# Performance work log

Measured on AMD Instinct MI355X. Metric: run time of the kernel, lower is better.

The kernel has to match this reference:

```python
import jax, jax.numpy as jnp
import numpy as np
import math

B, L, D, H, DFF = 8, 2048, 512, 8, 2048
FACTOR = 5

def setup_inputs() -> dict:
    key = jax.random.key(0)
    ks = jax.random.split(key, 20)
    r = lambda k, shape, s=0.02: (jax.random.normal(k, shape, jnp.float32) * s)
    return {
        'encoder_output': jax.random.normal(ks[0], (B, L, D), jnp.float32),
        'Wq': r(ks[1], (D, D)), 'bq': jnp.zeros((D,), jnp.float32),
        'Wk': r(ks[2], (D, D)), 'bk': jnp.zeros((D,), jnp.float32),
        'Wv': r(ks[3], (D, D)), 'bv': jnp.zeros((D,), jnp.float32),
        'Wo': r(ks[4], (D, D)), 'bo': jnp.zeros((D,), jnp.float32),
        'W1': r(ks[5], (DFF, D)), 'b1': jnp.zeros((DFF,), jnp.float32),
        'W2': r(ks[6], (D, DFF)), 'b2': jnp.zeros((D,), jnp.float32),
        'g1': jnp.ones((D,), jnp.float32), 'be1': jnp.zeros((D,), jnp.float32),
        'g2': jnp.ones((D,), jnp.float32), 'be2': jnp.zeros((D,), jnp.float32),
        'Wout': r(ks[7], (D, 1)), 'bout': jnp.zeros((1,), jnp.float32),
    }

def _layernorm(x, g, b, eps=1e-5):
    m = x.mean(-1, keepdims=True)
    v = x.var(-1, keepdims=True)
    return (x - m) / jnp.sqrt(v + eps) * g + b

def reference(encoder_output, Wq, bq, Wk, bk, Wv, bv, Wo, bo,
              W1, b1, W2, b2, g1, be1, g2, be2, Wout, bout):
    x = encoder_output  # [B, L, D]
    dh = D // H
    u = min(L, FACTOR * math.ceil(math.log(L)))  # number of active queries (static)

    # multi-head projections -> [B, H, L, dh]
    q = (x @ Wq + bq).reshape(B, L, H, dh).transpose(0, 2, 1, 3)
    k = (x @ Wk + bk).reshape(B, L, H, dh).transpose(0, 2, 1, 3)
    v = (x @ Wv + bv).reshape(B, L, H, dh).transpose(0, 2, 1, 3)

    # deterministic prob-sparse: sparsity measurement over all keys
    scores = jnp.einsum('bhld,bhsd->bhls', q, k) / math.sqrt(dh)  # [B,H,L,L]
    M = scores.max(-1) - scores.mean(-1)                           # [B,H,L]
    top_idx = jax.lax.top_k(M, u)[1]                               # [B,H,u]

    top_scores = jnp.take_along_axis(scores, top_idx[..., None], axis=2)  # [B,H,u,L]
    attn = jax.nn.softmax(top_scores, axis=-1)
    top_out = jnp.einsum('bhus,bhsd->bhud', attn, v)               # [B,H,u,dh]

    # lazy queries get mean(V); active queries get true attention
    ctx = jnp.broadcast_to(v.mean(axis=2, keepdims=True), (B, H, L, dh))
    bi = jnp.arange(B)[:, None, None]
    hi = jnp.arange(H)[None, :, None]
    ctx = ctx.at[bi, hi, top_idx].set(top_out)                     # [B,H,L,dh]

    attn_out = ctx.transpose(0, 2, 1, 3).reshape(B, L, D) @ Wo + bo  # [B,L,D]

    # decoder body: mean-pool, residual norms, pointwise conv FFN (eval-mode dropout = identity)
    a = attn_out.mean(axis=1)                 # [B, D]
    a = _layernorm(a + a, g1, be1)[:, None, :]  # [B, 1, D]  (a + dropout(a))

    ff = jax.nn.relu(a @ W1.T + b1)           # conv1d k=1 == linear, [B,1,DFF]
    ff = ff @ W2.T + b2                       # [B,1,D]
    out = _layernorm(a + ff, g2, be2)         # [B,1,D]

    forecasts = (out @ Wout + bout).squeeze(-1)  # [B,1]
    return forecasts, out
```

## Files before the change

### kernel.cpp

```cpp
#include <hip/hip_runtime.h>
#include <hip/hip_bf16.h>


#define B_   8
#define L_   2048
#define D_   512
#define H_   8
#define DH_  64
#define DFF_ 2048
#define U_   40
#define BH_  64
#define NM_  16384
#define NCK_ 16
#define CKS_ 128

typedef __bf16 bf16_t;
typedef __bf16 bf16x8 __attribute__((ext_vector_type(8)));
typedef float  f32x4  __attribute__((ext_vector_type(4)));

__device__ __forceinline__ void gl_lds16(const bf16_t* g, bf16_t* l) {
    __builtin_amdgcn_global_load_lds(
        (const __attribute__((address_space(1))) unsigned int*)g,
        (__attribute__((address_space(3))) unsigned int*)l, 16, 0, 0);
}

__global__ void k_cvt(const float* __restrict__ X, bf16_t* __restrict__ Xb) {
    size_t g = (size_t)blockIdx.x * 256 + threadIdx.x;
    const float4* xp = (const float4*)&X[g * 8];
    float4 f0 = xp[0], f1 = xp[1];
    bf16x8 hv;
    hv[0]=(bf16_t)f0.x; hv[1]=(bf16_t)f0.y; hv[2]=(bf16_t)f0.z; hv[3]=(bf16_t)f0.w;
    hv[4]=(bf16_t)f1.x; hv[5]=(bf16_t)f1.y; hv[6]=(bf16_t)f1.z; hv[7]=(bf16_t)f1.w;
    *(bf16x8*)&Xb[g * 8] = hv;
}

__global__ void k_transpose_w(const float* __restrict__ Wq, const float* __restrict__ Wk,
                              const float* __restrict__ Wv, bf16_t* __restrict__ WT) {
    __shared__ float tile[64][65];
    int blk = blockIdx.x;
    int mat = blk >> 6, tl = blk & 63;
    int tr = (tl >> 3) << 6;
    int tc = (tl & 7) << 6;
    const float* W = (mat == 0) ? Wq : (mat == 1) ? Wk : Wv;
    int t = threadIdx.x;
    #pragma unroll
    for (int i = 0; i < 16; ++i) {
        int e = t + i * 256, r = e >> 6, c = e & 63;
        tile[r][c] = W[(size_t)(tr + r) * 512 + tc + c];
    }
    __syncthreads();
    #pragma unroll
    for (int i = 0; i < 16; ++i) {
        int e = t + i * 256, r = e >> 6, c = e & 63;
        WT[(size_t)(mat * 512 + tc + r) * 512 + tr + c] = (bf16_t)tile[c][r];
    }
}

__global__ __launch_bounds__(256) void k_qkv(const bf16_t* __restrict__ Xb,
        const bf16_t* __restrict__ WT,
        const float* __restrict__ bq, const float* __restrict__ bk, const float* __restrict__ bv,
        bf16_t* __restrict__ Qb, bf16_t* __restrict__ Kb, float* __restrict__ Vf) {
    __shared__ bf16_t As[128 * 64];
    __shared__ bf16_t Bs[128 * 64];
    int t = threadIdx.x;
    int m0 = blockIdx.y * 128;
    int n0 = blockIdx.x * 128;
    int wv = t >> 6, lane = t & 63, lr = lane & 15, qd = lane >> 4;
    int wm = (wv & 1) * 64, wn = (wv >> 1) * 64;
    f32x4 acc[4][4];
    #pragma unroll
    for (int a = 0; a < 4; ++a)
        #pragma unroll
        for (int b = 0; b < 4; ++b) acc[a][b] = (f32x4){0.f, 0.f, 0.f, 0.f};

    for (int kt = 0; kt < 8; ++kt) {
        __syncthreads();
        #pragma unroll
        for (int i = 0; i < 4; ++i) {
            int ch = i * 256 + t, r = ch >> 3, c8 = ch & 7;
            gl_lds16(&Xb[(size_t)(m0 + r) * 512 + kt * 64 + c8 * 8], &As[ch * 8]);
        }
        #pragma unroll
        for (int i = 0; i < 4; ++i) {
            int ch = i * 256 + t, r = ch >> 3, c8 = ch & 7;
            gl_lds16(&WT[(size_t)(n0 + r) * 512 + kt * 64 + c8 * 8], &Bs[ch * 8]);
        }
        __syncthreads();
        bf16x8 af[4][2], bfg[4][2];
        #pragma unroll
        for (int rf = 0; rf < 4; ++rf)
            #pragma unroll
            for (int ks = 0; ks < 2; ++ks)
                af[rf][ks] = *(bf16x8*)&As[(wm + rf * 16 + lr) * 64 + ks * 32 + qd * 8];
        #pragma unroll
        for (int cf = 0; cf < 4; ++cf)
            #pragma unroll
            for (int ks = 0; ks < 2; ++ks)
                bfg[cf][ks] = *(bf16x8*)&Bs[(wn + cf * 16 + lr) * 64 + ks * 32 + qd * 8];
        #pragma unroll
        for (int cf = 0; cf < 4; ++cf)
            #pragma unroll
            for (int rf = 0; rf < 4; ++rf) {
                acc[rf][cf] = __builtin_amdgcn_mfma_f32_16x16x32_bf16(af[rf][0], bfg[cf][0], acc[rf][cf], 0, 0, 0);
                acc[rf][cf] = __builtin_amdgcn_mfma_f32_16x16x32_bf16(af[rf][1], bfg[cf][1], acc[rf][cf], 0, 0, 0);
            }
    }
    int sec = n0 >> 9;
    const float* bias = (sec == 0) ? bq : (sec == 1) ? bk : bv;
    #pragma unroll
    for (int rf = 0; rf < 4; ++rf) {
        #pragma unroll
        for (int r = 0; r < 4; ++r) {
            int m = m0 + wm + rf * 16 + qd * 4 + r;
            int b = m >> 11, l = m & 2047;
            #pragma unroll
            for (int cf = 0; cf < 4; ++cf) {
                int n = n0 + wn + cf * 16 + lr;
                int nn = n & 511;
                int h = nn >> 6, d = nn & 63;
                float val = acc[rf][cf][r] + bias[nn];
                size_t oidx = ((size_t)(b * 8 + h) * L_ + l) * 64 + d;
                if (sec == 0)      Qb[oidx] = (bf16_t)val;
                else if (sec == 1) Kb[oidx] = (bf16_t)val;
                else               Vf[oidx] = val;
            }
        }
    }
}

__global__ __launch_bounds__(256) void k_rowmax(const bf16_t* __restrict__ Qb,
        const bf16_t* __restrict__ Kb, float* __restrict__ rowmax) {
    __shared__ bf16_t Ks[128 * 64];
    int t = threadIdx.x;
    int bh = blockIdx.y;
    int row0 = blockIdx.x * 256;
    int wv = t >> 6, lane = t & 63, lr = lane & 15, qd = lane >> 4;
    size_t base = (size_t)bh * L_ * DH_;
    bf16x8 af[4][2];
    #pragma unroll
    for (int rf = 0; rf < 4; ++rf)
        #pragma unroll
        for (int ks = 0; ks < 2; ++ks)
            af[rf][ks] = *(const bf16x8*)&Qb[base + (size_t)(row0 + wv * 64 + rf * 16 + lr) * 64 + ks * 32 + qd * 8];
    float pmax[4][4];
    #pragma unroll
    for (int a = 0; a < 4; ++a)
        #pragma unroll
        for (int r = 0; r < 4; ++r) pmax[a][r] = -3.4e38f;

    for (int cb = 0; cb < 16; ++cb) {
        __syncthreads();
        #pragma unroll
        for (int i = 0; i < 4; ++i) {
            int ch = i * 256 + t, r = ch >> 3, c8 = ch & 7;
            gl_lds16(&Kb[base + (size_t)(cb * 128 + r) * 64 + c8 * 8], &Ks[ch * 8]);
        }
        __syncthreads();
        #pragma unroll
        for (int cf = 0; cf < 8; cf += 2) {
            bf16x8 bA0 = *(bf16x8*)&Ks[(cf * 16 + lr) * 64 + qd * 8];
            bf16x8 bA1 = *(bf16x8*)&Ks[(cf * 16 + lr) * 64 + 32 + qd * 8];
            bf16x8 bB0 = *(bf16x8*)&Ks[((cf + 1) * 16 + lr) * 64 + qd * 8];
            bf16x8 bB1 = *(bf16x8*)&Ks[((cf + 1) * 16 + lr) * 64 + 32 + qd * 8];
            #pragma unroll
            for (int rf = 0; rf < 4; ++rf) {
                f32x4 z = {0.f, 0.f, 0.f, 0.f};
                f32x4 c0 = __builtin_amdgcn_mfma_f32_16x16x32_bf16(af[rf][0], bA0, z, 0, 0, 0);
                c0 = __builtin_amdgcn_mfma_f32_16x16x32_bf16(af[rf][1], bA1, c0, 0, 0, 0);
                f32x4 c1 = __builtin_amdgcn_mfma_f32_16x16x32_bf16(af[rf][0], bB0, z, 0, 0, 0);
                c1 = __builtin_amdgcn_mfma_f32_16x16x32_bf16(af[rf][1], bB1, c1, 0, 0, 0);
                #pragma unroll
                for (int r = 0; r < 4; ++r)
                    pmax[rf][r] = fmaxf(pmax[rf][r], fmaxf(c0[r], c1[r]));
            }
        }
    }
    #pragma unroll
    for (int rf = 0; rf < 4; ++rf)
        #pragma unroll
        for (int r = 0; r < 4; ++r) {
            float v = pmax[rf][r];
            v = fmaxf(v, __shfl_xor(v, 1));
            v = fmaxf(v, __shfl_xor(v, 2));
            v = fmaxf(v, __shfl_xor(v, 4));
            v = fmaxf(v, __shfl_xor(v, 8));
            if (lr == 0)
                rowmax[bh * L_ + row0 + wv * 64 + rf * 16 + qd * 4 + r] = v;
        }
}

__global__ void k_sums(const bf16_t* __restrict__ Kb, const float* __restrict__ Vf,
                       float* __restrict__ kpart, float* __restrict__ vpart) {
    __shared__ float red[32][64];
    int t = threadIdx.x;
    int seg = blockIdx.x, bh = blockIdx.y;
    int d8 = t & 7, g = t >> 3;
    size_t base = (size_t)bh * L_ * DH_ + (size_t)seg * 256 * DH_;
    float s[8];
    #pragma unroll
    for (int j = 0; j < 8; ++j) s[j] = 0.f;
    #pragma unroll
    for (int ss = 0; ss < 8; ++ss) {
        bf16x8 kk = *(const bf16x8*)&Kb[base + (size_t)(g * 8 + ss) * 64 + d8 * 8];
        #pragma unroll
        for (int j = 0; j < 8; ++j) s[j] += (float)kk[j];
    }
    #pragma unroll
    for (int j = 0; j < 8; ++j) red[g][d8 * 8 + j] = s[j];
    __syncthreads();
    if (t < 64) {
        float a = 0.f;
        #pragma unroll
        for (int gg = 0; gg < 32; ++gg) a += red[gg][t];
        kpart[(bh * 8 + seg) * 64 + t] = a;
    }
    __syncthreads();
    #pragma unroll
    for (int j = 0; j < 8; ++j) s[j] = 0.f;
    #pragma unroll
    for (int ss = 0; ss < 8; ++ss) {
        const float4* vp = (const float4*)&Vf[base + (size_t)(g * 8 + ss) * 64 + d8 * 8];
        float4 v0 = vp[0], v1 = vp[1];
        s[0]+=v0.x; s[1]+=v0.y; s[2]+=v0.z; s[3]+=v0.w;
        s[4]+=v1.x; s[5]+=v1.y; s[6]+=v1.z; s[7]+=v1.w;
    }
    __syncthreads();
    #pragma unroll
    for (int j = 0; j < 8; ++j) red[g][d8 * 8 + j] = s[j];
    __syncthreads();
    if (t < 64) {
        float a = 0.f;
        #pragma unroll
        for (int gg = 0; gg < 32; ++gg) a += red[gg][t];
        vpart[(bh * 8 + seg) * 64 + t] = a;
    }
}

__global__ void k_M(const bf16_t* __restrict__ Qb, const float* __restrict__ rowmax,
                    const float* __restrict__ kpart, float* __restrict__ Mv) {
    __shared__ float ks_s[64];
    int t = threadIdx.x, blk = blockIdx.x;
    int bh = blk >> 3, lb = blk & 7;
    if (t < 64) {
        float a = 0.f;
        #pragma unroll
        for (int seg = 0; seg < 8; ++seg) a += kpart[(bh * 8 + seg) * 64 + t];
        ks_s[t] = a;
    }
    __syncthreads();
    int l = lb * 256 + t;
    const bf16x8* qp = (const bf16x8*)&Qb[((size_t)bh * L_ + l) * 64];
    float acc = 0.f;
    #pragma unroll
    for (int c8 = 0; c8 < 8; ++c8) {
        bf16x8 q8 = qp[c8];
        #pragma unroll
        for (int j = 0; j < 8; ++j) acc += (float)q8[j] * ks_s[c8 * 8 + j];
    }
    Mv[bh * L_ + l] = rowmax[bh * L_ + l] - acc * (1.0f / 2048.0f);
}

__global__ void k_topk(const float* __restrict__ Mv, int* __restrict__ topidx) {
    int lane = threadIdx.x;
    int bh = blockIdx.x;
    unsigned key[32];
    #pragma unroll
    for (int j = 0; j < 32; ++j) {
        unsigned b = __float_as_uint(Mv[bh * L_ + j * 64 + lane]);
        key[j] = (b & 0x80000000u) ? ~b : (b | 0x80000000u);
    }
    unsigned lo = 0u, hi = 0xFFFFFFFFu;
    while (lo < hi) {
        unsigned mid = lo + ((hi - lo) >> 1) + 1;
        int c = 0;
        #pragma unroll
        for (int j = 0; j < 32; ++j)
            c += __popcll(__ballot(key[j] >= mid));
        if (c >= U_) lo = mid; else hi = mid - 1;
    }
    unsigned K40 = lo;
    int c_gt = 0;
    #pragma unroll
    for (int j = 0; j < 32; ++j)
        c_gt += __popcll(__ballot(key[j] > K40));
    unsigned long long lmask = (1ull << lane) - 1ull;
    int base_gt = 0, base_eq = 0;
    #pragma unroll
    for (int j = 0; j < 32; ++j) {
        bool gt = key[j] > K40, eq = key[j] == K40;
        unsigned long long mg = __ballot(gt);
        unsigned long long me = __ballot(eq);
        if (gt) {
            int pos = base_gt + __popcll(mg & lmask);
            topidx[bh * U_ + pos] = j * 64 + lane;
        } else if (eq) {
            int ep = base_eq + __popcll(me & lmask);
            if (c_gt + ep < U_)
                topidx[bh * U_ + c_gt + ep] = j * 64 + lane;
        }
        base_gt += __popcll(mg);
        base_eq += __popcll(me);
    }
}

__global__ __launch_bounds__(256) void k_attn2(const bf16_t* __restrict__ Qb,
        const bf16_t* __restrict__ Kb, const float* __restrict__ Vf,
        const int* __restrict__ topidx, float* __restrict__ part) {
    __shared__ bf16_t Qs[48 * 72];
    __shared__ bf16_t Ks[128 * 64];
    __shared__ bf16_t Vt[64 * 136];
    __shared__ float  wred[4][48];
    __shared__ float  frow[48];
    __shared__ int    tid_s[40];
    bf16_t* Ps = Ks;

    int t = threadIdx.x;
    int ck = blockIdx.x, bh = blockIdx.y;
    int c0 = ck * CKS_;
    size_t base = (size_t)bh * L_ * DH_;
    if (t < 40) tid_s[t] = topidx[bh * U_ + t];
    __syncthreads();
    #pragma unroll
    for (int i = 0; i < 4; ++i) {
        int s = i * 256 + t, r = s >> 3, cs = s & 7, c = cs ^ (r & 7);
        gl_lds16(&Kb[base + (size_t)(c0 + r) * 64 + c * 8], &Ks[s * 8]);
    }
    for (int e = t; e < 48 * 8; e += 256) {
        int r = e >> 3, c8 = e & 7;
        bf16x8 v;
        #pragma unroll
        for (int j = 0; j < 8; ++j) v[j] = (bf16_t)0.f;
        if (r < 40) v = *(const bf16x8*)&Qb[base + (size_t)tid_s[r] * 64 + c8 * 8];
        *(bf16x8*)&Qs[r * 72 + c8 * 8] = v;
    }
    #pragma unroll
    for (int i = 0; i < 8; ++i) {
        int e = t + i * 256;
        int key = e >> 4, d4 = e & 15;
        float4 v = *(const float4*)&Vf[base + (size_t)(c0 + key) * 64 + d4 * 4];
        Vt[(d4 * 4 + 0) * 136 + key] = (bf16_t)v.x;
        Vt[(d4 * 4 + 1) * 136 + key] = (bf16_t)v.y;
        Vt[(d4 * 4 + 2) * 136 + key] = (bf16_t)v.z;
        Vt[(d4 * 4 + 3) * 136 + key] = (bf16_t)v.w;
    }
    __syncthreads();

    int wv = t >> 6, lane = t & 63, lr = lane & 15, qd = lane >> 4;
    bf16x8 aq[3][2];
    #pragma unroll
    for (int tm = 0; tm < 3; ++tm)
        #pragma unroll
        for (int ks = 0; ks < 2; ++ks)
            aq[tm][ks] = *(bf16x8*)&Qs[(tm * 16 + lr) * 72 + ks * 32 + qd * 8];
    f32x4 S[3][2];
    #pragma unroll
    for (int nt = 0; nt < 2; ++nt) {
        int key = wv * 32 + nt * 16 + lr;
        bf16x8 bk0 = *(bf16x8*)&Ks[key * 64 + ((qd ^ (key & 7)) * 8)];
        bf16x8 bk1 = *(bf16x8*)&Ks[key * 64 + (((4 + qd) ^ (key & 7)) * 8)];
        #pragma unroll
        for (int tm = 0; tm < 3; ++tm) {
            f32x4 z = {0.f, 0.f, 0.f, 0.f};
            z = __builtin_amdgcn_mfma_f32_16x16x32_bf16(aq[tm][0], bk0, z, 0, 0, 0);
            S[tm][nt] = __builtin_amdgcn_mfma_f32_16x16x32_bf16(aq[tm][1], bk1, z, 0, 0, 0);
        }
    }
    float rm[3][4];
    #pragma unroll
    for (int tm = 0; tm < 3; ++tm)
        #pragma unroll
        for (int r = 0; r < 4; ++r) {
            float v = fmaxf(S[tm][0][r], S[tm][1][r]);
            v = fmaxf(v, __shfl_xor(v, 1));
            v = fmaxf(v, __shfl_xor(v, 2));
            v = fmaxf(v, __shfl_xor(v, 4));
            v = fmaxf(v, __shfl_xor(v, 8));
            rm[tm][r] = v;
        }
    if (lr == 0) {
        #pragma unroll
        for (int tm = 0; tm < 3; ++tm)
            #pragma unroll
            for (int r = 0; r < 4; ++r)
                wred[wv][tm * 16 + qd * 4 + r] = rm[tm][r];
    }
    __syncthreads();
    if (t < 48)
        frow[t] = fmaxf(fmaxf(wred[0][t], wred[1][t]), fmaxf(wred[2][t], wred[3][t]));
    __syncthreads();
    float rs_[3][4];
    #pragma unroll
    for (int tm = 0; tm < 3; ++tm) {
        #pragma unroll
        for (int r = 0; r < 4; ++r) {
            float fm = frow[tm * 16 + qd * 4 + r];
            float s0 = __expf((S[tm][0][r] - fm) * 0.125f);
            float s1 = __expf((S[tm][1][r] - fm) * 0.125f);
            Ps[(tm * 16 + qd * 4 + r) * 136 + wv * 32 + lr]      = (bf16_t)s0;
            Ps[(tm * 16 + qd * 4 + r) * 136 + wv * 32 + 16 + lr] = (bf16_t)s1;
            rs_[tm][r] = s0 + s1;
        }
    }
    #pragma unroll
    for (int tm = 0; tm < 3; ++tm)
        #pragma unroll
        for (int r = 0; r < 4; ++r) {
            float v = rs_[tm][r];
            v += __shfl_xor(v, 1);
            v += __shfl_xor(v, 2);
            v += __shfl_xor(v, 4);
            v += __shfl_xor(v, 8);
            rs_[tm][r] = v;
        }
    if (lr == 0) {
        #pragma unroll
        for (int tm = 0; tm < 3; ++tm)
            #pragma unroll
            for (int r = 0; r < 4; ++r)
                wred[wv][tm * 16 + qd * 4 + r] = rs_[tm][r];
    }
    __syncthreads();
    float* pb = &part[(((size_t)bh * NCK_ + ck) * 40) * 66];
    if (t < 40) {
        pb[t * 66 + 64] = frow[t] * 0.125f;
        pb[t * 66 + 65] = wred[0][t] + wred[1][t] + wred[2][t] + wred[3][t];
    }
    f32x4 O[3];
    #pragma unroll
    for (int tm = 0; tm < 3; ++tm) O[tm] = (f32x4){0.f, 0.f, 0.f, 0.f};
    #pragma unroll
    for (int kk = 0; kk < 4; ++kk) {
        bf16x8 bv = *(bf16x8*)&Vt[(wv * 16 + lr) * 136 + kk * 32 + qd * 8];
        #pragma unroll
        for (int tm = 0; tm < 3; ++tm) {
            bf16x8 ap = *(bf16x8*)&Ps[(tm * 16 + lr) * 136 + kk * 32 + qd * 8];
            O[tm] = __builtin_amdgcn_mfma_f32_16x16x32_bf16(ap, bv, O[tm], 0, 0, 0);
        }
    }
    #pragma unroll
    for (int tm = 0; tm < 3; ++tm)
        #pragma unroll
        for (int r = 0; r < 4; ++r) {
            int row = tm * 16 + qd * 4 + r;
            if (row < 40) pb[row * 66 + wv * 16 + lr] = O[tm][r];
        }
}

__global__ void k_attnred(const float* __restrict__ part, float* __restrict__ tout) {
    int t = threadIdx.x, bh = blockIdx.x;
    int d = t & 63, rg = t >> 6;
    const float* pb0 = &part[((size_t)bh * NCK_) * 40 * 66];
    for (int ri = 0; ri < 10; ++ri) {
        int r = rg + 4 * ri;
        float M = -3.4e38f;
        #pragma unroll
        for (int c = 0; c < NCK_; ++c) M = fmaxf(M, pb0[(c * 40 + r) * 66 + 64]);
        float lsum = 0.f, osum = 0.f;
        #pragma unroll
        for (int c = 0; c < NCK_; ++c) {
            float w = __expf(pb0[(c * 40 + r) * 66 + 64] - M);
            lsum += w * pb0[(c * 40 + r) * 66 + 65];
            osum += w * pb0[(c * 40 + r) * 66 + d];
        }
        tout[((size_t)bh * U_ + r) * 64 + d] = osum / lsum;
    }
}

__global__ void k_ctx(const float* __restrict__ vpart, const float* __restrict__ topout,
                      const float* __restrict__ Wo, const float* __restrict__ bo,
                      const float* __restrict__ g1, const float* __restrict__ be1,
                      float* __restrict__ a2) {
    __shared__ float cm[512];
    __shared__ float rs[256], rq[256];
    int t = threadIdx.x, b = blockIdx.x;
    #pragma unroll
    for (int p = 0; p < 2; ++p) {
        int hd = t + p * 256;
        int h = hd >> 6, dd = hd & 63;
        int bh = b * 8 + h;
        float vs = 0.f;
        #pragma unroll
        for (int seg = 0; seg < 8; ++seg) vs += vpart[(bh * 8 + seg) * 64 + dd];
        float tsum = 0.f;
        for (int ii = 0; ii < U_; ++ii) tsum += topout[((size_t)bh * U_ + ii) * 64 + dd];
        cm[hd] = (0.98046875f * vs + tsum) * (1.0f / 2048.0f);
    }
    __syncthreads();
    float x[2];
    #pragma unroll
    for (int p = 0; p < 2; ++p) {
        int j = t + p * 256;
        float acc = bo[j];
        for (int c = 0; c < 128; ++c) {
            float4 cv = *(const float4*)&cm[c * 4];
            acc += cv.x * Wo[(size_t)(c * 4 + 0) * 512 + j];
            acc += cv.y * Wo[(size_t)(c * 4 + 1) * 512 + j];
            acc += cv.z * Wo[(size_t)(c * 4 + 2) * 512 + j];
            acc += cv.w * Wo[(size_t)(c * 4 + 3) * 512 + j];
        }
        x[p] = 2.0f * acc;
    }
    rs[t] = x[0] + x[1];
    rq[t] = x[0] * x[0] + x[1] * x[1];
    __syncthreads();
    for (int str = 128; str > 0; str >>= 1) {
        if (t < str) { rs[t] += rs[t + str]; rq[t] += rq[t + str]; }
        __syncthreads();
    }
    float mean = rs[0] * (1.0f / 512.0f);
    float var  = rq[0] * (1.0f / 512.0f) - mean * mean;
    float rstd = rsqrtf(var + 1e-5f);
    #pragma unroll
    for (int p = 0; p < 2; ++p) {
        int j = t + p * 256;
        a2[b * 512 + j] = (x[p] - mean) * rstd * g1[j] + be1[j];
    }
}

__global__ void k_ff1p(const float* __restrict__ a2, const float* __restrict__ W1,
                       float* __restrict__ ffp) {
    __shared__ float Ws[64 * 132];
    __shared__ float as[8 * 128];
    int t = threadIdx.x;
    int jb = blockIdx.x, seg = blockIdx.y;
    int j0 = jb * 64, c0 = seg * 128;
    #pragma unroll
    for (int i = 0; i < 8; ++i) {
        int e = t + i * 256;
        int r = e >> 5, c4 = e & 31;
        *(float4*)&Ws[r * 132 + c4 * 4] =
            *(const float4*)&W1[(size_t)(j0 + r) * 512 + c0 + c4 * 4];
    }
    for (int e = t; e < 1024; e += 256) {
        int b = e >> 7, c = e & 127;
        as[b * 128 + c] = a2[b * 512 + c0 + c];
    }
    __syncthreads();
    int j = t & 63, bp = t >> 6;
    float acc0 = 0.f, acc1 = 0.f;
    for (int c = 0; c < 32; ++c) {
        float4 w  = *(float4*)&Ws[j * 132 + c * 4];
        float4 xa = *(float4*)&as[(bp * 2) * 128 + c * 4];
        float4 xb = *(float4*)&as[(bp * 2 + 1) * 128 + c * 4];
        acc0 += w.x * xa.x + w.y * xa.y + w.z * xa.z + w.w * xa.w;
        acc1 += w.x * xb.x + w.y * xb.y + w.z * xb.z + w.w * xb.w;
    }
    ffp[(size_t)(seg * 8 + bp * 2) * 2048 + j0 + j]     = acc0;
    ffp[(size_t)(seg * 8 + bp * 2 + 1) * 2048 + j0 + j] = acc1;
}

__global__ void k_ffr(const float* __restrict__ ffp, const float* __restrict__ b1v,
                      float* __restrict__ ffb) {
    int e = blockIdx.x * 256 + threadIdx.x;
    int b = e >> 11, j = e & 2047;
    float s = b1v[j];
    #pragma unroll
    for (int seg = 0; seg < 4; ++seg) s += ffp[(size_t)(seg * 8 + b) * 2048 + j];
    ffb[b * 2048 + j] = fmaxf(s, 0.f);
}

__global__ void k_ff2p(const float* __restrict__ ffb, const float* __restrict__ W2,
                       float* __restrict__ ff2p) {
    __shared__ float Ws[32 * 260];
    __shared__ float fs[8 * 256];
    int t = threadIdx.x;
    int db = blockIdx.x, seg = blockIdx.y;
    int d0 = db * 32, c0 = seg * 256;
    #pragma unroll
    for (int i = 0; i < 8; ++i) {
        int e = t + i * 256;
        int r = e >> 6, c4 = e & 63;
        *(float4*)&Ws[r * 260 + c4 * 4] =
            *(const float4*)&W2[(size_t)(d0 + r) * 2048 + c0 + c4 * 4];
    }
    for (int e = t; e < 2048; e += 256) {
        int b = e >> 8, c = e & 255;
        fs[b * 256 + c] = ffb[b * 2048 + c0 + c];
    }
    __syncthreads();
    int d = t & 31, b = t >> 5;
    float acc = 0.f;
    for (int c = 0; c < 64; ++c) {
        float4 w = *(float4*)&Ws[d * 260 + c * 4];
        float4 x = *(float4*)&fs[b * 256 + c * 4];
        acc += w.x * x.x + w.y * x.y + w.z * x.z + w.w * x.w;
    }
    ff2p[(size_t)(seg * 8 + b) * 512 + d0 + d] = acc;
}

__global__ void k_final(const float* __restrict__ a2, const float* __restrict__ ff2p,
                        const float* __restrict__ b2v,
                        const float* __restrict__ g2, const float* __restrict__ be2,
                        const float* __restrict__ Wout, const float* __restrict__ bout,
                        float* __restrict__ dout) {
    __shared__ float rs[256], rq[256];
    int t = threadIdx.x, b = blockIdx.x;
    float f0 = b2v[t], f1 = b2v[t + 256];
    #pragma unroll
    for (int seg = 0; seg < 8; ++seg) {
        f0 += ff2p[(size_t)(seg * 8 + b) * 512 + t];
        f1 += ff2p[(size_t)(seg * 8 + b) * 512 + t + 256];
    }
    float x0 = a2[b * 512 + t] + f0;
    float x1 = a2[b * 512 + t + 256] + f1;
    rs[t] = x0 + x1;
    rq[t] = x0 * x0 + x1 * x1;
    __syncthreads();
    for (int str = 128; str > 0; str >>= 1) {
        if (t < str) { rs[t] += rs[t + str]; rq[t] += rq[t + str]; }
        __syncthreads();
    }
    float mean = rs[0] * (1.0f / 512.0f);
    float var  = rq[0] * (1.0f / 512.0f) - mean * mean;
    float rstd = rsqrtf(var + 1e-5f);
    float o0 = (x0 - mean) * rstd * g2[t]       + be2[t];
    float o1 = (x1 - mean) * rstd * g2[t + 256] + be2[t + 256];
    dout[8 + b * 512 + t]       = o0;
    dout[8 + b * 512 + t + 256] = o1;
    __syncthreads();
    rs[t] = o0 * Wout[t] + o1 * Wout[t + 256];
    __syncthreads();
    for (int str = 128; str > 0; str >>= 1) {
        if (t < str) rs[t] += rs[t + str];
        __syncthreads();
    }
    if (t == 0) dout[b] = rs[0] + bout[0];
}

extern "C" void kernel_launch(void* const* d_in, const int* in_sizes, int n_in,
                              void* d_out, int out_size, void* d_ws, size_t ws_size,
                              hipStream_t stream) {
    const float* X    = (const float*)d_in[0];
    const float* Wq   = (const float*)d_in[1];
    const float* bq   = (const float*)d_in[2];
    const float* Wk   = (const float*)d_in[3];
    const float* bk   = (const float*)d_in[4];
    const float* Wv   = (const float*)d_in[5];
    const float* bv   = (const float*)d_in[6];
    const float* Wo   = (const float*)d_in[7];
    const float* bo   = (const float*)d_in[8];
    const float* W1   = (const float*)d_in[9];
    const float* b1   = (const float*)d_in[10];
    const float* W2   = (const float*)d_in[11];
    const float* b2   = (const float*)d_in[12];
    const float* g1   = (const float*)d_in[13];
    const float* be1  = (const float*)d_in[14];
    const float* g2   = (const float*)d_in[15];
    const float* be2  = (const float*)d_in[16];
    const float* Wout = (const float*)d_in[17];
    const float* bout = (const float*)d_in[18];
    float* out = (float*)d_out;

    char* ws = (char*)d_ws;
    size_t off = 0;
    auto alloc = [&](size_t bytes) -> void* {
        void* p = ws + off;
        off += (bytes + 255) & ~(size_t)255;
        return p;
    };
    bf16_t* Xb   = (bf16_t*)alloc((size_t)NM_ * D_ * 2);
    bf16_t* WT   = (bf16_t*)alloc((size_t)1536 * 512 * 2);
    bf16_t* Qb   = (bf16_t*)alloc((size_t)BH_ * L_ * DH_ * 2);
    bf16_t* Kb   = (bf16_t*)alloc((size_t)BH_ * L_ * DH_ * 2);
    float*  Vf   = (float*) alloc((size_t)BH_ * L_ * DH_ * 4);
    float*  rmx  = (float*) alloc((size_t)BH_ * L_ * 4);
    float*  Mv   = (float*) alloc((size_t)BH_ * L_ * 4);
    float*  kpart= (float*) alloc((size_t)BH_ * 8 * 64 * 4);
    float*  vpart= (float*) alloc((size_t)BH_ * 8 * 64 * 4);
    int*    tidx = (int*)   alloc((size_t)BH_ * U_ * 4);
    float*  tout = (float*) alloc((size_t)BH_ * U_ * 64 * 4);
    float*  a2   = (float*) alloc(8 * 512 * 4);
    float*  ffp  = (float*) alloc((size_t)4 * 8 * 2048 * 4);
    float*  ffb  = (float*) alloc(8 * 2048 * 4);
    float*  ff2p = (float*) alloc((size_t)8 * 8 * 512 * 4);
    float*  part = (float*)Xb;
    (void)ws_size; (void)in_sizes; (void)n_in; (void)out_size;

    hipLaunchKernelGGL(k_cvt,         dim3(4096),       dim3(256), 0, stream, X, Xb);
    hipLaunchKernelGGL(k_transpose_w, dim3(192),        dim3(256), 0, stream, Wq, Wk, Wv, WT);
    hipLaunchKernelGGL(k_qkv,         dim3(12, 128),    dim3(256), 0, stream, Xb, WT, bq, bk, bv, Qb, Kb, Vf);
    hipLaunchKernelGGL(k_rowmax,      dim3(8, 64),      dim3(256), 0, stream, Qb, Kb, rmx);
    hipLaunchKernelGGL(k_sums,        dim3(8, 64),      dim3(256), 0, stream, Kb, Vf, kpart, vpart);
    hipLaunchKernelGGL(k_M,           dim3(512),        dim3(256), 0, stream, Qb, rmx, kpart, Mv);
    hipLaunchKernelGGL(k_topk,        dim3(64),         dim3(64),  0, stream, Mv, tidx);
    hipLaunchKernelGGL(k_attn2,       dim3(NCK_, 64),   dim3(256), 0, stream, Qb, Kb, Vf, tidx, part);
    hipLaunchKernelGGL(k_attnred,     dim3(64),         dim3(256), 0, stream, part, tout);
    hipLaunchKernelGGL(k_ctx,         dim3(8),          dim3(256), 0, stream, vpart, tout, Wo, bo, g1, be1, a2);
    hipLaunchKernelGGL(k_ff1p,        dim3(32, 4),      dim3(256), 0, stream, a2, W1, ffp);
    hipLaunchKernelGGL(k_ffr,         dim3(64),         dim3(256), 0, stream, ffp, b1, ffb);
    hipLaunchKernelGGL(k_ff2p,        dim3(16, 8),      dim3(256), 0, stream, ffb, W2, ff2p);
    hipLaunchKernelGGL(k_final,       dim3(8),          dim3(256), 0, stream, a2, ff2p, b2, g2, be2, Wout, bout, out);
}
```

Before: 320.1 us.

## Fuse sparsity measure into rowmax kernel, swizzle K LDS, halve rows per block

```diff
diff --git a/kernel.cpp b/kernel.cpp
--- a/kernel.cpp
+++ b/kernel.cpp
@@ -129,22 +129,44 @@
 }
 
 __global__ __launch_bounds__(256) void k_rowmax(const bf16_t* __restrict__ Qb,
-        const bf16_t* __restrict__ Kb, float* __restrict__ rowmax) {
+        const bf16_t* __restrict__ Kb, const float* __restrict__ kpart,
+        float* __restrict__ Mv) {
     __shared__ bf16_t Ks[128 * 64];
+    __shared__ float ksum_s[64];
+    __shared__ float dot_s[128];
     int t = threadIdx.x;
     int bh = blockIdx.y;
-    int row0 = blockIdx.x * 256;
+    int row0 = blockIdx.x * 128;
     int wv = t >> 6, lane = t & 63, lr = lane & 15, qd = lane >> 4;
     size_t base = (size_t)bh * L_ * DH_;
-    bf16x8 af[4][2];
-    #pragma unroll
-    for (int rf = 0; rf < 4; ++rf)
+    if (t < 64) {
+        float a = 0.f;
+        #pragma unroll
+        for (int seg = 0; seg < 8; ++seg) a += kpart[(bh * 8 + seg) * 64 + t];
+        ksum_s[t] = a;
+    }
+    bf16x8 af[2][2];
+    #pragma unroll
+    for (int rf = 0; rf < 2; ++rf)
         #pragma unroll
         for (int ks = 0; ks < 2; ++ks)
-            af[rf][ks] = *(const bf16x8*)&Qb[base + (size_t)(row0 + wv * 64 + rf * 16 + lr) * 64 + ks * 32 + qd * 8];
-    float pmax[4][4];
-    #pragma unroll
-    for (int a = 0; a < 4; ++a)
+            af[rf][ks] = *(const bf16x8*)&Qb[base + (size_t)(row0 + wv * 32 + rf * 16 + lr) * 64 + ks * 32 + qd * 8];
+    __syncthreads();
+    #pragma unroll
+    for (int rf = 0; rf < 2; ++rf) {
+        float v = 0.f;
+        #pragma unroll
+        for (int ks = 0; ks < 2; ++ks)
+            #pragma unroll
+            for (int j = 0; j < 8; ++j)
+                v += (float)af[rf][ks][j] * ksum_s[ks * 32 + qd * 8 + j];
+        v += __shfl_xor(v, 16);
+        v += __shfl_xor(v, 32);
+        if (qd == 0) dot_s[wv * 32 + rf * 16 + lr] = v;
+    }
+    float pmax[2][4];
+    #pragma unroll
+    for (int a = 0; a < 2; ++a)
         #pragma unroll
         for (int r = 0; r < 4; ++r) pmax[a][r] = -3.4e38f;
 
@@ -152,18 +174,19 @@
         __syncthreads();
         #pragma unroll
         for (int i = 0; i < 4; ++i) {
-            int ch = i * 256 + t, r = ch >> 3, c8 = ch & 7;
-            gl_lds16(&Kb[base + (size_t)(cb * 128 + r) * 64 + c8 * 8], &Ks[ch * 8]);
+            int s = i * 256 + t, r = s >> 3, cs = s & 7, c = cs ^ (r & 7);
+            gl_lds16(&Kb[base + (size_t)(cb * 128 + r) * 64 + c * 8], &Ks[s * 8]);
         }
         __syncthreads();
         #pragma unroll
         for (int cf = 0; cf < 8; cf += 2) {
-            bf16x8 bA0 = *(bf16x8*)&Ks[(cf * 16 + lr) * 64 + qd * 8];
-            bf16x8 bA1 = *(bf16x8*)&Ks[(cf * 16 + lr) * 64 + 32 + qd * 8];
-            bf16x8 bB0 = *(bf16x8*)&Ks[((cf + 1) * 16 + lr) * 64 + qd * 8];
-            bf16x8 bB1 = *(bf16x8*)&Ks[((cf + 1) * 16 + lr) * 64 + 32 + qd * 8];
-            #pragma unroll
-            for (int rf = 0; rf < 4; ++rf) {
+            int keyA = cf * 16 + lr, keyB = (cf + 1) * 16 + lr;
+            bf16x8 bA0 = *(bf16x8*)&Ks[keyA * 64 + ((qd ^ (keyA & 7)) * 8)];
+            bf16x8 bA1 = *(bf16x8*)&Ks[keyA * 64 + (((4 + qd) ^ (keyA & 7)) * 8)];
+            bf16x8 bB0 = *(bf16x8*)&Ks[keyB * 64 + ((qd ^ (keyB & 7)) * 8)];
+            bf16x8 bB1 = *(bf16x8*)&Ks[keyB * 64 + (((4 + qd) ^ (keyB & 7)) * 8)];
+            #pragma unroll
+            for (int rf = 0; rf < 2; ++rf) {
                 f32x4 z = {0.f, 0.f, 0.f, 0.f};
                 f32x4 c0 = __builtin_amdgcn_mfma_f32_16x16x32_bf16(af[rf][0], bA0, z, 0, 0, 0);
                 c0 = __builtin_amdgcn_mfma_f32_16x16x32_bf16(af[rf][1], bA1, c0, 0, 0, 0);
@@ -176,7 +199,7 @@
         }
     }
     #pragma unroll
-    for (int rf = 0; rf < 4; ++rf)
+    for (int rf = 0; rf < 2; ++rf)
         #pragma unroll
         for (int r = 0; r < 4; ++r) {
             float v = pmax[rf][r];
@@ -184,8 +207,10 @@
             v = fmaxf(v, __shfl_xor(v, 2));
             v = fmaxf(v, __shfl_xor(v, 4));
             v = fmaxf(v, __shfl_xor(v, 8));
-            if (lr == 0)
-                rowmax[bh * L_ + row0 + wv * 64 + rf * 16 + qd * 4 + r] = v;
+            if (lr == 0) {
+                int row = wv * 32 + rf * 16 + qd * 4 + r;
+                Mv[bh * L_ + row0 + row] = v - dot_s[row] * (1.0f / 2048.0f);
+            }
         }
 }
 
@@ -234,30 +259,6 @@
         for (int gg = 0; gg < 32; ++gg) a += red[gg][t];
         vpart[(bh * 8 + seg) * 64 + t] = a;
     }
-}
-
-__global__ void k_M(const bf16_t* __restrict__ Qb, const float* __restrict__ rowmax,
-                    const float* __restrict__ kpart, float* __restrict__ Mv) {
-    __shared__ float ks_s[64];
-    int t = threadIdx.x, blk = blockIdx.x;
-    int bh = blk >> 3, lb = blk & 7;
-    if (t < 64) {
-        float a = 0.f;
-        #pragma unroll
-        for (int seg = 0; seg < 8; ++seg) a += kpart[(bh * 8 + seg) * 64 + t];
-        ks_s[t] = a;
-    }
-    __syncthreads();
-    int l = lb * 256 + t;
-    const bf16x8* qp = (const bf16x8*)&Qb[((size_t)bh * L_ + l) * 64];
-    float acc = 0.f;
-    #pragma unroll
-    for (int c8 = 0; c8 < 8; ++c8) {
-        bf16x8 q8 = qp[c8];
-        #pragma unroll
-        for (int j = 0; j < 8; ++j) acc += (float)q8[j] * ks_s[c8 * 8 + j];
-    }
-    Mv[bh * L_ + l] = rowmax[bh * L_ + l] - acc * (1.0f / 2048.0f);
 }
 
 __global__ void k_topk(const float* __restrict__ Mv, int* __restrict__ topidx) {
@@ -663,7 +664,6 @@
     bf16_t* Qb   = (bf16_t*)alloc((size_t)BH_ * L_ * DH_ * 2);
     bf16_t* Kb   = (bf16_t*)alloc((size_t)BH_ * L_ * DH_ * 2);
     float*  Vf   = (float*) alloc((size_t)BH_ * L_ * DH_ * 4);
-    float*  rmx  = (float*) alloc((size_t)BH_ * L_ * 4);
     float*  Mv   = (float*) alloc((size_t)BH_ * L_ * 4);
     float*  kpart= (float*) alloc((size_t)BH_ * 8 * 64 * 4);
     float*  vpart= (float*) alloc((size_t)BH_ * 8 * 64 * 4);
@@ -679,9 +679,8 @@
     hipLaunchKernelGGL(k_cvt,         dim3(4096),       dim3(256), 0, stream, X, Xb);
     hipLaunchKernelGGL(k_transpose_w, dim3(192),        dim3(256), 0, stream, Wq, Wk, Wv, WT);
     hipLaunchKernelGGL(k_qkv,         dim3(12, 128),    dim3(256), 0, stream, Xb, WT, bq, bk, bv, Qb, Kb, Vf);
-    hipLaunchKernelGGL(k_rowmax,      dim3(8, 64),      dim3(256), 0, stream, Qb, Kb, rmx);
     hipLaunchKernelGGL(k_sums,        dim3(8, 64),      dim3(256), 0, stream, Kb, Vf, kpart, vpart);
-    hipLaunchKernelGGL(k_M,           dim3(512),        dim3(256), 0, stream, Qb, rmx, kpart, Mv);
+    hipLaunchKernelGGL(k_rowmax,      dim3(16, 64),     dim3(256), 0, stream, Qb, Kb, kpart, Mv);
     hipLaunchKernelGGL(k_topk,        dim3(64),         dim3(64),  0, stream, Mv, tidx);
     hipLaunchKernelGGL(k_attn2,       dim3(NCK_, 64),   dim3(256), 0, stream, Qb, Kb, Vf, tidx, part);
     hipLaunchKernelGGL(k_attnred,     dim3(64),         dim3(256), 0, stream, part, tout);
```

Measured after the change: 308.3 us. -3.7%, faster.
